# Optimization experiments

Measured on AMD Instinct MI355X. Metric: run time of the kernel, lower is better.

The kernel has to match this reference:

```python
import jax, jax.numpy as jnp
import numpy as np

B, H, W, C, HEADS, WS, SS = 32, 56, 56, 512, 16, 7, 3
HID = 4 * C
N = WS * WS          # tokens per window = 49
NW = (H // WS) * (W // WS)  # windows per image = 64
HD = C // HEADS
SCALE = HD ** -0.5

def _rel_index():
    coords = np.stack(np.meshgrid(np.arange(WS), np.arange(WS), indexing='ij'))
    cf = coords.reshape(2, -1)
    rel = (cf[:, :, None] - cf[:, None, :]).transpose(1, 2, 0)
    rel[..., 0] += WS - 1
    rel[..., 1] += WS - 1
    rel[..., 0] *= 2 * WS - 1
    return rel.sum(-1)  # [N, N]

REL_IDX = _rel_index()

def _attn_mask():
    # standard Swin SW-MSA mask: label 3x3 shifted regions, diff labels -> -100
    img = np.zeros((H, W), dtype=np.float32)
    cnt = 0
    for hs in (slice(0, -WS), slice(-WS, -SS), slice(-SS, None)):
        for ws_ in (slice(0, -WS), slice(-WS, -SS), slice(-SS, None)):
            img[hs, ws_] = cnt
            cnt += 1
    mw = img.reshape(H // WS, WS, W // WS, WS).transpose(0, 2, 1, 3).reshape(NW, N)
    diff = mw[:, None, :] - mw[:, :, None]
    return jnp.asarray(np.where(diff != 0, -100.0, 0.0).astype(np.float32))  # [NW, N, N]

ATTN_MASK = _attn_mask()

def layernorm(x, g, b, eps=1e-5):
    m = jnp.mean(x, -1, keepdims=True)
    v = jnp.mean((x - m) ** 2, -1, keepdims=True)
    return (x - m) * jax.lax.rsqrt(v + eps) * g + b

def setup_inputs():
    key = jax.random.key(0)
    ks = jax.random.split(key, 8)
    f32 = jnp.float32
    return {
        'x': jax.random.normal(ks[0], (B, H * W, C), f32),
        'norm1_g': jnp.ones((C,), f32), 'norm1_b': jnp.zeros((C,), f32),
        'qkv_w': jax.random.normal(ks[1], (3 * C, C), f32) * 0.02,
        'qkv_b': jnp.zeros((3 * C,), f32),
        'rel_bias': jax.random.normal(ks[2], ((2 * WS - 1) ** 2, HEADS), f32) * 0.02,
        'proj_w': jax.random.normal(ks[3], (C, C), f32) * 0.02,
        'proj_b': jnp.zeros((C,), f32),
        'norm2_g': jnp.ones((C,), f32), 'norm2_b': jnp.zeros((C,), f32),
        'mlp_w1': jax.random.normal(ks[4], (HID, C), f32) * 0.02,
        'mlp_b1': jnp.zeros((HID,), f32),
        'mlp_w2': jax.random.normal(ks[5], (C, HID), f32) * 0.02,
        'mlp_b2': jnp.zeros((C,), f32),
    }

def reference(x, norm1_g, norm1_b, qkv_w, qkv_b, rel_bias, proj_w, proj_b,
              norm2_g, norm2_b, mlp_w1, mlp_b1, mlp_w2, mlp_b2):
    skip = x
    h = layernorm(x, norm1_g, norm1_b).reshape(B, H, W, C)
    h = jnp.roll(h, (-SS, -SS), axis=(1, 2))  # cyclic shift
    # window partition -> [B*NW, N, C]
    h = h.reshape(B, H // WS, WS, W // WS, WS, C).transpose(0, 1, 3, 2, 4, 5).reshape(B * NW, N, C)
    qkv = (h @ qkv_w.T + qkv_b).reshape(B * NW, N, 3, HEADS, HD).transpose(2, 0, 3, 1, 4)
    q, k, v = qkv[0] * SCALE, qkv[1], qkv[2]  # [B*NW, HEADS, N, HD]
    attn = jnp.einsum('whnd,whmd->whnm', q, k)
    bias = rel_bias[REL_IDX.reshape(-1)].reshape(N, N, HEADS).transpose(2, 0, 1)
    attn = attn + bias[None]
    attn = attn.reshape(B, NW, HEADS, N, N) + ATTN_MASK[None, :, None]
    attn = jax.nn.softmax(attn, axis=-1).reshape(B * NW, HEADS, N, N)
    h = jnp.einsum('whnm,whmd->whnd', attn, v).transpose(0, 2, 1, 3).reshape(B * NW, N, C)
    h = h @ proj_w.T + proj_b
    # window reverse + reverse cyclic shift
    h = h.reshape(B, H // WS, W // WS, WS, WS, C).transpose(0, 1, 3, 2, 4, 5).reshape(B, H, W, C)
    h = jnp.roll(h, (SS, SS), axis=(1, 2)).reshape(B, H * W, C)
    x = skip + h
    m = layernorm(x, norm2_g, norm2_b)
    m = jax.nn.gelu(m @ mlp_w1.T + mlp_b1, approximate=False) @ mlp_w2.T + mlp_b2
    return x + m
```

## Files before the change

### kernel.cpp

```cpp
#include <hip/hip_runtime.h>
#include <cstdint>
#include <cstddef>

#define DI __device__ __forceinline__

typedef __bf16 bf16_t;
typedef __bf16 bf16x8 __attribute__((ext_vector_type(8)));
typedef float f32x4 __attribute__((ext_vector_type(4)));

static constexpr float SCALE = 0.17677669529663687f;

DI bf16_t f2b(float f) {
  uint32_t u = __builtin_bit_cast(uint32_t, f);
  u += 0x7fffu + ((u >> 16) & 1u);
  return __builtin_bit_cast(bf16_t, (uint16_t)(u >> 16));
}

DI void gld16(const void* g, void* l) {
  __builtin_amdgcn_global_load_lds(
      (const __attribute__((address_space(1))) uint32_t*)g,
      (__attribute__((address_space(3))) uint32_t*)l, 16, 0, 0);
}

__global__ __launch_bounds__(256)
void cvtw(const float* __restrict__ in, bf16_t* __restrict__ out, int n) {
  int i = (blockIdx.x * 256 + threadIdx.x) * 4;
  if (i >= n) return;
  float4 v = *(const float4*)(in + i);
  ushort4 o;
  o.x = __builtin_bit_cast(uint16_t, f2b(v.x));
  o.y = __builtin_bit_cast(uint16_t, f2b(v.y));
  o.z = __builtin_bit_cast(uint16_t, f2b(v.z));
  o.w = __builtin_bit_cast(uint16_t, f2b(v.w));
  *(ushort4*)(out + i) = o;
}

__global__ __launch_bounds__(256)
void bias_pre(const float* __restrict__ rel, float* __restrict__ bf) {
  int idx = blockIdx.x * 256 + threadIdx.x;
  int head = idx >> 12, t1 = (idx >> 6) & 63, t2 = idx & 63;
  float v = -1e30f;
  if (t1 < 49 && t2 < 49) {
    int i1 = t1 / 7, j1 = t1 - i1 * 7, i2 = t2 / 7, j2 = t2 - i2 * 7;
    v = rel[((i1 - i2 + 6) * 13 + (j1 - j2 + 6)) * 16 + head];
  }
  bf[idx] = v;
}

template<bool WIN>
__global__ __launch_bounds__(128)
void ln_kernel(const float* __restrict__ in, const float* __restrict__ g,
               const float* __restrict__ be, bf16_t* __restrict__ out)
{
  const int r = blockIdx.x;
  const int tid = threadIdx.x;
  long srow;
  if (WIN) {
    int bw = r / 49, t = r - bw * 49;
    int b = bw >> 6, w = bw & 63;
    int wh = w >> 3, ww = w & 7;
    int i = t / 7, j = t - i * 7;
    int hs = wh * 7 + i + 3; if (hs >= 56) hs -= 56;
    int wsr = ww * 7 + j + 3; if (wsr >= 56) wsr -= 56;
    srow = (long)b * 3136 + hs * 56 + wsr;
  } else {
    srow = r;
  }
  const float4 v = *(const float4*)(in + srow * 512 + tid * 4);
  float s = v.x + v.y + v.z + v.w;
  float sq = v.x * v.x + v.y * v.y + v.z * v.z + v.w * v.w;
#pragma unroll
  for (int m = 1; m < 64; m <<= 1) { s += __shfl_xor(s, m); sq += __shfl_xor(sq, m); }
  __shared__ float ls[2], lq[2];
  if ((tid & 63) == 0) { ls[tid >> 6] = s; lq[tid >> 6] = sq; }
  __syncthreads();
  s = ls[0] + ls[1]; sq = lq[0] + lq[1];
  const float mean = s * (1.f / 512.f);
  const float rs = rsqrtf(sq * (1.f / 512.f) - mean * mean + 1e-5f);
  const float4 gg = *(const float4*)(g + tid * 4);
  const float4 bb = *(const float4*)(be + tid * 4);
  ushort4 o;
  o.x = __builtin_bit_cast(uint16_t, f2b((v.x - mean) * rs * gg.x + bb.x));
  o.y = __builtin_bit_cast(uint16_t, f2b((v.y - mean) * rs * gg.y + bb.y));
  o.z = __builtin_bit_cast(uint16_t, f2b((v.z - mean) * rs * gg.z + bb.z));
  o.w = __builtin_bit_cast(uint16_t, f2b((v.w - mean) * rs * gg.w + bb.w));
  *(ushort4*)(out + (long)r * 512 + tid * 4) = o;
}

#define MFMA16(a, b, c) __builtin_amdgcn_mfma_f32_16x16x32_bf16((a), (b), (c), 0, 0, 0)

template<int EPI>
__global__ __launch_bounds__(512, 2)
void gemm256(const bf16_t* __restrict__ A, const bf16_t* __restrict__ Bw,
             const float* __restrict__ bias, const float* __restrict__ extra,
             void* __restrict__ out0, void* __restrict__ out1v, void* __restrict__ out2v,
             const int K, const int NBN)
{
  __shared__ __align__(128) bf16_t lds[8][8192];
  const int tid = threadIdx.x, lane = tid & 63, wave = tid >> 6;

  const int nwg = gridDim.x;
  const int q = nwg >> 3, r = nwg & 7;
  const int xcd = blockIdx.x & 7, sidx = blockIdx.x >> 3;
  const int wgid = (xcd < r ? xcd * (q + 1) : r * (q + 1) + (xcd - r) * q) + sidx;
  const int bm = wgid / NBN, bn = wgid - bm * NBN;

  const int srow = tid >> 2, slot = tid & 3;
  const int chunk = slot ^ ((srow >> 1) & 3);
  const bf16_t* pA = A + (size_t)(bm * 256 + srow) * K + chunk * 8;
  const bf16_t* pB = Bw + (size_t)(bn * 256 + srow) * K + chunk * 8;
  const size_t rowK = (size_t)128 * K;
  const int NT = K >> 6;

#define STG(mat, b, h, koff) do { \
    const bf16_t* _p = ((mat) ? pB : pA) + (koff); \
    bf16_t* _l = &lds[((mat) ? 4 : 0) + (b) * 2 + (h)][tid * 8]; \
    gld16(_p, _l); \
    gld16(_p + rowK, _l + 4096); \
  } while (0)

  STG(0, 0, 0, 0);  STG(1, 0, 0, 0);
  STG(0, 0, 1, 32); STG(1, 0, 1, 32);
  STG(0, 1, 0, 64); STG(1, 1, 0, 64);
  STG(0, 1, 1, 96);

  const int fr = lane & 15, fkc = lane >> 4;
  const int wr = wave >> 2, wc = wave & 3;
  const int slotq = (fkc ^ ((fr >> 1) & 3)) << 3;
  const int aoff = (wr * 128 + fr) * 32 + slotq;
  const int boff = (wc * 64 + fr) * 32 + slotq;

  f32x4 acc[8][4] = {};
  bf16x8 af[8], bq[4];

  asm volatile("s_waitcnt vmcnt(6)");
  __builtin_amdgcn_s_barrier();
  __builtin_amdgcn_sched_barrier(0);

#define PH_SYNC() \
  __builtin_amdgcn_sched_barrier(0); \
  __builtin_amdgcn_s_barrier(); \
  asm volatile("s_waitcnt lgkmcnt(0)"); \
  __builtin_amdgcn_sched_barrier(0); \
  __builtin_amdgcn_s_setprio(1)

#define PH_END() \
  __builtin_amdgcn_s_setprio(0); \
  __builtin_amdgcn_sched_barrier(0); \
  __builtin_amdgcn_s_barrier()

#define MM2(N0, N1) \
  _Pragma("unroll") \
  for (int m = 0; m < 8; ++m) { \
    acc[m][N0] = MFMA16(af[m], bq[N0], acc[m][N0]); \
    acc[m][N1] = MFMA16(af[m], bq[N1], acc[m][N1]); \
  }

#define KTILE(B, KT) do { \
     \
    _Pragma("unroll") \
    for (int m = 0; m < 8; ++m) af[m] = *(const bf16x8*)&lds[(B) * 2][aoff + m * 512]; \
    bq[0] = *(const bf16x8*)&lds[4 + (B) * 2][boff]; \
    bq[1] = *(const bf16x8*)&lds[4 + (B) * 2][boff + 512]; \
    if ((KT) + 1 < NT) STG(1, (B) ^ 1, 1, ((KT) + 1) * 64 + 32); \
    PH_SYNC(); \
    MM2(0, 1); \
    PH_END(); \
     \
    bq[2] = *(const bf16x8*)&lds[4 + (B) * 2][boff + 1024]; \
    bq[3] = *(const bf16x8*)&lds[4 + (B) * 2][boff + 1536]; \
    if ((KT) + 2 < NT) STG(0, (B), 0, ((KT) + 2) * 64); \
    PH_SYNC(); \
    MM2(2, 3); \
    PH_END(); \
     \
    _Pragma("unroll") \
    for (int m = 0; m < 8; ++m) af[m] = *(const bf16x8*)&lds[(B) * 2 + 1][aoff + m * 512]; \
    bq[0] = *(const bf16x8*)&lds[4 + (B) * 2 + 1][boff]; \
    bq[1] = *(const bf16x8*)&lds[4 + (B) * 2 + 1][boff + 512]; \
    if ((KT) + 2 < NT) STG(1, (B), 0, ((KT) + 2) * 64); \
    PH_SYNC(); \
    MM2(0, 1); \
    PH_END(); \
     \
    bq[2] = *(const bf16x8*)&lds[4 + (B) * 2 + 1][boff + 1024]; \
    bq[3] = *(const bf16x8*)&lds[4 + (B) * 2 + 1][boff + 1536]; \
    if ((KT) + 2 < NT) STG(0, (B), 1, ((KT) + 2) * 64 + 32); \
    PH_SYNC(); \
    MM2(2, 3); \
    __builtin_amdgcn_s_setprio(0); \
    __builtin_amdgcn_sched_barrier(0); \
    if ((KT) + 2 < NT) asm volatile("s_waitcnt vmcnt(6)"); \
    else               asm volatile("s_waitcnt vmcnt(0)"); \
    __builtin_amdgcn_s_barrier(); \
    __builtin_amdgcn_sched_barrier(0); \
  } while (0)

  for (int kt = 0; kt < NT; kt += 2) {
    KTILE(0, kt);
    KTILE(1, kt + 1);
  }
#undef KTILE
#undef MM2
#undef PH_END
#undef PH_SYNC
#undef STG

  const int rq = fkc * 4;
  float bs[4];
#pragma unroll
  for (int n = 0; n < 4; ++n) bs[n] = bias[bn * 256 + wc * 64 + n * 16 + fr];

#pragma unroll
  for (int m = 0; m < 8; ++m) {
#pragma unroll
    for (int j = 0; j < 4; ++j) {
      const int grow = bm * 256 + wr * 128 + m * 16 + rq + j;
      long obase = 0;
      if (EPI == 0) {
        int bwi = grow / 49, t = grow - bwi * 49;
        obase = ((long)bwi * 784 + t) * 32;
      } else if (EPI == 1) {
        int bwi = grow / 49, t = grow - bwi * 49;
        int b = bwi >> 6, w = bwi & 63;
        int wh = w >> 3, ww = w & 7;
        int i = t / 7, jj = t - i * 7;
        int hs = wh * 7 + i + 3; if (hs >= 56) hs -= 56;
        int wsr = ww * 7 + jj + 3; if (wsr >= 56) wsr -= 56;
        obase = ((long)b * 3136 + hs * 56 + wsr) * 512;
      } else if (EPI == 2) {
        obase = (long)grow * 2048;
      } else {
        obase = (long)grow * 512;
      }
#pragma unroll
      for (int n = 0; n < 4; ++n) {
        const int gcol = bn * 256 + wc * 64 + n * 16 + fr;
        float v = acc[m][n][j] + bs[n];
        if (EPI == 0) {
          int part = gcol >> 9, head = (gcol >> 5) & 15, d = gcol & 31;
          if (part == 0) v *= SCALE;
          bf16_t* dst = (bf16_t*)(part == 0 ? out0 : (part == 1 ? out1v : out2v));
          dst[obase + (long)head * 1568 + d] = f2b(v);
        } else if (EPI == 1) {
          ((float*)out0)[obase + gcol] = v + extra[obase + gcol];
        } else if (EPI == 2) {
          float m2 = v * v;
          float z = v * fmaf(0.07135481627f, m2, 1.59576912161f);
          float e = __expf(z);
          float rr = __builtin_amdgcn_rcpf(e + 1.0f);
          ((bf16_t*)out0)[obase + gcol] = f2b(fmaf(-v, rr, v));
        } else {
          ((float*)out0)[obase + gcol] = v + extra[obase + gcol];
        }
      }
    }
  }
}

__global__ __launch_bounds__(256)
void attn_kernel(const bf16_t* __restrict__ qb, const bf16_t* __restrict__ kb,
                 const bf16_t* __restrict__ vb, const float* __restrict__ biasf,
                 bf16_t* __restrict__ aout)
{
  __shared__ bf16_t Q[64 * 32];
  __shared__ bf16_t Kl[64 * 32];
  __shared__ bf16_t Vt[32 * 64];
  __shared__ bf16_t Pl[4][16 * 64];
  const int bid = blockIdx.x;
  const int bw = bid >> 4, head = bid & 15;
  const int tid = threadIdx.x, lane = tid & 63, wave = tid >> 6;
  {
    uint4 z = {0u, 0u, 0u, 0u};
    *(uint4*)&Q[tid * 8] = z;
    *(uint4*)&Kl[tid * 8] = z;
    *(uint4*)&Vt[tid * 8] = z;
  }
  __syncthreads();
  const bf16_t* qsrc = qb + (long)bid * (49 * 32);
  const bf16_t* ksrc = kb + (long)bid * (49 * 32);
  const bf16_t* vsrc = vb + (long)bid * (49 * 32);
  if (tid < 196) {
    *(uint4*)&Q[tid * 8] = *(const uint4*)(qsrc + tid * 8);
    *(uint4*)&Kl[tid * 8] = *(const uint4*)(ksrc + tid * 8);
  }
  for (int e = tid; e < 1568; e += 256) {
    int t = e >> 5, d = e & 31;
    Vt[d * 64 + t] = vsrc[e];
  }
  __syncthreads();
  const int fr = lane & 15, fk = (lane >> 4) * 8, rq = (lane >> 4) * 4;
  bf16x8 aq = *(const bf16x8*)&Q[(wave * 16 + fr) * 32 + fk];
  f32x4 s[4];
#pragma unroll
  for (int n = 0; n < 4; ++n) {
    bf16x8 bk = *(const bf16x8*)&Kl[(n * 16 + fr) * 32 + fk];
    f32x4 z = {0.f, 0.f, 0.f, 0.f};
    s[n] = __builtin_amdgcn_mfma_f32_16x16x32_bf16(aq, bk, z, 0, 0, 0);
  }
  const int w = bw & 63;
  const bool wh7 = ((w >> 3) == 7), ww7 = ((w & 7) == 7);
  const float* bh = biasf + head * 4096;
#pragma unroll
  for (int j = 0; j < 4; ++j) {
    const int row = wave * 16 + rq + j;
    int i1 = row / 7, j1 = row - i1 * 7;
    bool b1h = wh7 && (i1 >= 4), b1w = ww7 && (j1 >= 4);
    float pv[4];
    float mx = -3.0e38f;
#pragma unroll
    for (int n = 0; n < 4; ++n) {
      const int col = n * 16 + fr;
      float v = s[n][j] + bh[row * 64 + col];
      if (wh7 || ww7) {
        int i2 = col / 7, j2 = col - i2 * 7;
        bool b2h = wh7 && (i2 >= 4), b2w = ww7 && (j2 >= 4);
        if ((b1h != b2h) || (b1w != b2w)) v -= 100.f;
      }
      pv[n] = v;
      mx = fmaxf(mx, v);
    }
#pragma unroll
    for (int msk = 1; msk < 16; msk <<= 1) mx = fmaxf(mx, __shfl_xor(mx, msk));
    float sm = 0.f;
#pragma unroll
    for (int n = 0; n < 4; ++n) { pv[n] = __expf(pv[n] - mx); sm += pv[n]; }
#pragma unroll
    for (int msk = 1; msk < 16; msk <<= 1) sm += __shfl_xor(sm, msk);
    const float inv = 1.f / sm;
#pragma unroll
    for (int n = 0; n < 4; ++n)
      Pl[wave][(rq + j) * 64 + n * 16 + fr] = f2b(pv[n] * inv);
  }
  __syncthreads();
  f32x4 o[2] = {};
#pragma unroll
  for (int kk = 0; kk < 2; ++kk) {
    bf16x8 pa = *(const bf16x8*)&Pl[wave][fr * 64 + kk * 32 + fk];
#pragma unroll
    for (int dt = 0; dt < 2; ++dt) {
      bf16x8 vv = *(const bf16x8*)&Vt[(dt * 16 + fr) * 64 + kk * 32 + fk];
      o[dt] = __builtin_amdgcn_mfma_f32_16x16x32_bf16(pa, vv, o[dt], 0, 0, 0);
    }
  }
#pragma unroll
  for (int j = 0; j < 4; ++j) {
    const int t1 = wave * 16 + rq + j;
    if (t1 < 49) {
      bf16_t* dst = aout + ((long)bw * 49 + t1) * 512 + head * 32;
      dst[fr] = f2b(o[0][j]);
      dst[16 + fr] = f2b(o[1][j]);
    }
  }
}

extern "C" void kernel_launch(void* const* d_in, const int* in_sizes, int n_in,
                              void* d_out, int out_size, void* d_ws, size_t ws_size,
                              hipStream_t stream)
{
  const float* x      = (const float*)d_in[0];
  const float* n1g    = (const float*)d_in[1];
  const float* n1b    = (const float*)d_in[2];
  const float* qkv_w  = (const float*)d_in[3];
  const float* qkv_b  = (const float*)d_in[4];
  const float* rel    = (const float*)d_in[5];
  const float* proj_w = (const float*)d_in[6];
  const float* proj_b = (const float*)d_in[7];
  const float* n2g    = (const float*)d_in[8];
  const float* n2b    = (const float*)d_in[9];
  const float* w1     = (const float*)d_in[10];
  const float* b1     = (const float*)d_in[11];
  const float* w2     = (const float*)d_in[12];
  const float* b2     = (const float*)d_in[13];

  char* ws = (char*)d_ws;
  bf16_t* Wqkv  = (bf16_t*)(ws + 0);
  bf16_t* Wproj = (bf16_t*)(ws + 1572864);
  bf16_t* Wm1   = (bf16_t*)(ws + 2097152);
  bf16_t* Wm2   = (bf16_t*)(ws + 4194304);
  float*  biasf = (float*)(ws + 6291456);
  const size_t ABYTES = (size_t)100352 * 512 * 2;
  const size_t P1 = 8388608;
  const size_t P2 = P1 + ABYTES + 1048576;
  bf16_t* xw      = (bf16_t*)(ws + P1);
  bf16_t* qbuf    = (bf16_t*)(ws + P2);
  bf16_t* kbuf    = (bf16_t*)(ws + P2 + ABYTES);
  bf16_t* vbuf    = (bf16_t*)(ws + P2 + 2 * ABYTES);
  bf16_t* attnout = xw;
  bf16_t* h2      = xw;
  bf16_t* hidden  = qbuf;

  cvtw<<<768, 256, 0, stream>>>(qkv_w, Wqkv, 1536 * 512);
  cvtw<<<256, 256, 0, stream>>>(proj_w, Wproj, 512 * 512);
  cvtw<<<1024, 256, 0, stream>>>(w1, Wm1, 2048 * 512);
  cvtw<<<1024, 256, 0, stream>>>(w2, Wm2, 512 * 2048);
  bias_pre<<<256, 256, 0, stream>>>(rel, biasf);

  ln_kernel<true><<<100352, 128, 0, stream>>>(x, n1g, n1b, xw);
  gemm256<0><<<392 * 6, 512, 0, stream>>>(xw, Wqkv, qkv_b, nullptr,
                                          qbuf, kbuf, vbuf, 512, 6);
  attn_kernel<<<32768, 256, 0, stream>>>(qbuf, kbuf, vbuf, biasf, attnout);
  gemm256<1><<<392 * 2, 512, 0, stream>>>(attnout, Wproj, proj_b, x,
                                          d_out, nullptr, nullptr, 512, 2);
  ln_kernel<false><<<100352, 128, 0, stream>>>((const float*)d_out, n2g, n2b, h2);
  gemm256<2><<<392 * 8, 512, 0, stream>>>(h2, Wm1, b1, nullptr,
                                          hidden, nullptr, nullptr, 512, 8);
  gemm256<3><<<392 * 2, 512, 0, stream>>>(hidden, Wm2, b2, (const float*)d_out,
                                          d_out, nullptr, nullptr, 2048, 2);
}
```

Measured before the change: 1.356 ms.

## Make GEMMs persistent with contiguous tile ranges and cross-tile prefetch

All four GEMM launches now run a fixed grid of 256 workgroups, each taking a contiguous range of 256x256 output tiles mapped so that workgroups on the same XCD are adjacent. The LDS staging pipeline continues across tile boundaries, so loads for the next tile's K slices are issued while the current tile finishes and runs its epilogue. This targets wave-quantization tails and per-tile pipeline fill/drain. With launch bounds allowing 2 blocks per CU, 256 blocks may leave CUs idle, and the epilogue is serialized inside the loop.

```diff
diff --git a/kernel.cpp b/kernel.cpp
--- a/kernel.cpp
+++ b/kernel.cpp
@@ -98,31 +98,47 @@
 {
   __shared__ __align__(128) bf16_t lds[8][8192];
   const int tid = threadIdx.x, lane = tid & 63, wave = tid >> 6;
-
-  const int nwg = gridDim.x;
-  const int q = nwg >> 3, r = nwg & 7;
+  const int NT = K >> 6;
+  const int ntiles = NBN * 392;
+
   const int xcd = blockIdx.x & 7, sidx = blockIdx.x >> 3;
-  const int wgid = (xcd < r ? xcd * (q + 1) : r * (q + 1) + (xcd - r) * q) + sidx;
-  const int bm = wgid / NBN, bn = wgid - bm * NBN;
+  const int c = xcd * 32 + sidx;
+  const int q2 = ntiles >> 8, r2 = ntiles & 255;
+  const int t0 = c * q2 + (c < r2 ? c : r2);
+  const int t1 = t0 + q2 + (c < r2 ? 1 : 0);
 
   const int srow = tid >> 2, slot = tid & 3;
   const int chunk = slot ^ ((srow >> 1) & 3);
-  const bf16_t* pA = A + (size_t)(bm * 256 + srow) * K + chunk * 8;
-  const bf16_t* pB = Bw + (size_t)(bn * 256 + srow) * K + chunk * 8;
   const size_t rowK = (size_t)128 * K;
-  const int NT = K >> 6;
-
-#define STG(mat, b, h, koff) do { \
-    const bf16_t* _p = ((mat) ? pB : pA) + (koff); \
-    bf16_t* _l = &lds[((mat) ? 4 : 0) + (b) * 2 + (h)][tid * 8]; \
-    gld16(_p, _l); \
-    gld16(_p + rowK, _l + 4096); \
+  const size_t PANEL = (size_t)256 * K;
+
+  int bmC = t0 / NBN, bnC = t0 - bmC * NBN;
+
+  const bf16_t* pAs = A + (size_t)(bmC * 256 + srow) * K + chunk * 8;
+  const bf16_t* pBs = Bw + (size_t)(bnC * 256 + srow) * K + chunk * 8;
+  int hA = 0, hB = 0, ktA = 0, hhA = 0, bnA = bnC, ktB = 0, hhB = 0, bnB = bnC;
+  const int ST = (t1 - t0) * NT;
+  const int hEnd = ST * 2;
+
+#define STG_A() do { \
+    if (hA < hEnd) { \
+      const bf16_t* _p = pAs + ktA * 64 + hhA * 32; \
+      bf16_t* _l = &lds[(ktA & 1) * 2 + hhA][tid * 8]; \
+      gld16(_p, _l); gld16(_p + rowK, _l + 4096); \
+      ++hA; hhA ^= 1; \
+      if (!hhA) { if (++ktA == NT) { ktA = 0; if (++bnA == NBN) { bnA = 0; pAs += PANEL; } } } \
+    } \
   } while (0)
 
-  STG(0, 0, 0, 0);  STG(1, 0, 0, 0);
-  STG(0, 0, 1, 32); STG(1, 0, 1, 32);
-  STG(0, 1, 0, 64); STG(1, 1, 0, 64);
-  STG(0, 1, 1, 96);
+#define STG_B() do { \
+    if (hB < hEnd) { \
+      const bf16_t* _p = pBs + ktB * 64 + hhB * 32; \
+      bf16_t* _l = &lds[4 + (ktB & 1) * 2 + hhB][tid * 8]; \
+      gld16(_p, _l); gld16(_p + rowK, _l + 4096); \
+      ++hB; hhB ^= 1; \
+      if (!hhB) { if (++ktB == NT) { ktB = 0; pBs += PANEL; if (++bnB == NBN) { bnB = 0; pBs -= (size_t)NBN * PANEL; } } } \
+    } \
+  } while (0)
 
   const int fr = lane & 15, fkc = lane >> 4;
   const int wr = wave >> 2, wc = wave & 3;
@@ -133,6 +149,7 @@
   f32x4 acc[8][4] = {};
   bf16x8 af[8], bq[4];
 
+  STG_A(); STG_B(); STG_A(); STG_B(); STG_A(); STG_B(); STG_A();
   asm volatile("s_waitcnt vmcnt(6)");
   __builtin_amdgcn_s_barrier();
   __builtin_amdgcn_sched_barrier(0);
@@ -156,20 +173,20 @@
     acc[m][N1] = MFMA16(af[m], bq[N1], acc[m][N1]); \
   }
 
-#define KTILE(B, KT) do { \
+#define KTILE(B) do { \
      \
     _Pragma("unroll") \
     for (int m = 0; m < 8; ++m) af[m] = *(const bf16x8*)&lds[(B) * 2][aoff + m * 512]; \
     bq[0] = *(const bf16x8*)&lds[4 + (B) * 2][boff]; \
     bq[1] = *(const bf16x8*)&lds[4 + (B) * 2][boff + 512]; \
-    if ((KT) + 1 < NT) STG(1, (B) ^ 1, 1, ((KT) + 1) * 64 + 32); \
+    STG_B(); \
     PH_SYNC(); \
     MM2(0, 1); \
     PH_END(); \
      \
     bq[2] = *(const bf16x8*)&lds[4 + (B) * 2][boff + 1024]; \
     bq[3] = *(const bf16x8*)&lds[4 + (B) * 2][boff + 1536]; \
-    if ((KT) + 2 < NT) STG(0, (B), 0, ((KT) + 2) * 64); \
+    STG_A(); \
     PH_SYNC(); \
     MM2(2, 3); \
     PH_END(); \
@@ -178,84 +195,95 @@
     for (int m = 0; m < 8; ++m) af[m] = *(const bf16x8*)&lds[(B) * 2 + 1][aoff + m * 512]; \
     bq[0] = *(const bf16x8*)&lds[4 + (B) * 2 + 1][boff]; \
     bq[1] = *(const bf16x8*)&lds[4 + (B) * 2 + 1][boff + 512]; \
-    if ((KT) + 2 < NT) STG(1, (B), 0, ((KT) + 2) * 64); \
+    STG_B(); \
     PH_SYNC(); \
     MM2(0, 1); \
     PH_END(); \
      \
     bq[2] = *(const bf16x8*)&lds[4 + (B) * 2 + 1][boff + 1024]; \
     bq[3] = *(const bf16x8*)&lds[4 + (B) * 2 + 1][boff + 1536]; \
-    if ((KT) + 2 < NT) STG(0, (B), 1, ((KT) + 2) * 64 + 32); \
+    STG_A(); \
     PH_SYNC(); \
     MM2(2, 3); \
     __builtin_amdgcn_s_setprio(0); \
     __builtin_amdgcn_sched_barrier(0); \
-    if ((KT) + 2 < NT) asm volatile("s_waitcnt vmcnt(6)"); \
-    else               asm volatile("s_waitcnt vmcnt(0)"); \
+    if (sG + 2 < ST) asm volatile("s_waitcnt vmcnt(6)"); \
+    else             asm volatile("s_waitcnt vmcnt(0)"); \
     __builtin_amdgcn_s_barrier(); \
     __builtin_amdgcn_sched_barrier(0); \
+    ++sG; \
   } while (0)
 
-  for (int kt = 0; kt < NT; kt += 2) {
-    KTILE(0, kt);
-    KTILE(1, kt + 1);
+  int sG = 0;
+  const int rq = fkc * 4;
+  for (int t = t0; t < t1; ++t) {
+#pragma unroll 1
+    for (int k2 = 0; k2 < NT; k2 += 2) {
+      KTILE(0);
+      KTILE(1);
+    }
+    {
+      float bs[4];
+#pragma unroll
+      for (int n = 0; n < 4; ++n) bs[n] = bias[bnC * 256 + wc * 64 + n * 16 + fr];
+#pragma unroll
+      for (int m = 0; m < 8; ++m) {
+#pragma unroll
+        for (int j = 0; j < 4; ++j) {
+          const int grow = bmC * 256 + wr * 128 + m * 16 + rq + j;
+          long obase = 0;
+          if (EPI == 0) {
+            int bwi = grow / 49, t_ = grow - bwi * 49;
+            obase = ((long)bwi * 784 + t_) * 32;
+          } else if (EPI == 1) {
+            int bwi = grow / 49, t_ = grow - bwi * 49;
+            int b = bwi >> 6, w = bwi & 63;
+            int wh = w >> 3, ww = w & 7;
+            int i = t_ / 7, jj = t_ - i * 7;
+            int hs = wh * 7 + i + 3; if (hs >= 56) hs -= 56;
+            int wsr = ww * 7 + jj + 3; if (wsr >= 56) wsr -= 56;
+            obase = ((long)b * 3136 + hs * 56 + wsr) * 512;
+          } else if (EPI == 2) {
+            obase = (long)grow * 2048;
+          } else {
+            obase = (long)grow * 512;
+          }
+#pragma unroll
+          for (int n = 0; n < 4; ++n) {
+            const int gcol = bnC * 256 + wc * 64 + n * 16 + fr;
+            float v = acc[m][n][j] + bs[n];
+            if (EPI == 0) {
+              int part = gcol >> 9, head = (gcol >> 5) & 15, d = gcol & 31;
+              if (part == 0) v *= SCALE;
+              bf16_t* dst = (bf16_t*)(part == 0 ? out0 : (part == 1 ? out1v : out2v));
+              dst[obase + (long)head * 1568 + d] = f2b(v);
+            } else if (EPI == 1) {
+              ((float*)out0)[obase + gcol] = v + extra[obase + gcol];
+            } else if (EPI == 2) {
+              float m2 = v * v;
+              float z = v * fmaf(0.07135481627f, m2, 1.59576912161f);
+              float e = __expf(z);
+              float rr = __builtin_amdgcn_rcpf(e + 1.0f);
+              ((bf16_t*)out0)[obase + gcol] = f2b(fmaf(-v, rr, v));
+            } else {
+              ((float*)out0)[obase + gcol] = v + extra[obase + gcol];
+            }
+          }
+        }
+      }
+#pragma unroll
+      for (int m = 0; m < 8; ++m)
+#pragma unroll
+        for (int n = 0; n < 4; ++n) acc[m][n] = (f32x4){0.f, 0.f, 0.f, 0.f};
+    }
+    if (++bnC == NBN) { bnC = 0; ++bmC; }
   }
 #undef KTILE
 #undef MM2
 #undef PH_END
 #undef PH_SYNC
-#undef STG
-
-  const int rq = fkc * 4;
-  float bs[4];
-#pragma unroll
-  for (int n = 0; n < 4; ++n) bs[n] = bias[bn * 256 + wc * 64 + n * 16 + fr];
-
-#pragma unroll
-  for (int m = 0; m < 8; ++m) {
-#pragma unroll
-    for (int j = 0; j < 4; ++j) {
-      const int grow = bm * 256 + wr * 128 + m * 16 + rq + j;
-      long obase = 0;
-      if (EPI == 0) {
-        int bwi = grow / 49, t = grow - bwi * 49;
-        obase = ((long)bwi * 784 + t) * 32;
-      } else if (EPI == 1) {
-        int bwi = grow / 49, t = grow - bwi * 49;
-        int b = bwi >> 6, w = bwi & 63;
-        int wh = w >> 3, ww = w & 7;
-        int i = t / 7, jj = t - i * 7;
-        int hs = wh * 7 + i + 3; if (hs >= 56) hs -= 56;
-        int wsr = ww * 7 + jj + 3; if (wsr >= 56) wsr -= 56;
-        obase = ((long)b * 3136 + hs * 56 + wsr) * 512;
-      } else if (EPI == 2) {
-        obase = (long)grow * 2048;
-      } else {
-        obase = (long)grow * 512;
-      }
-#pragma unroll
-      for (int n = 0; n < 4; ++n) {
-        const int gcol = bn * 256 + wc * 64 + n * 16 + fr;
-        float v = acc[m][n][j] + bs[n];
-        if (EPI == 0) {
-          int part = gcol >> 9, head = (gcol >> 5) & 15, d = gcol & 31;
-          if (part == 0) v *= SCALE;
-          bf16_t* dst = (bf16_t*)(part == 0 ? out0 : (part == 1 ? out1v : out2v));
-          dst[obase + (long)head * 1568 + d] = f2b(v);
-        } else if (EPI == 1) {
-          ((float*)out0)[obase + gcol] = v + extra[obase + gcol];
-        } else if (EPI == 2) {
-          float m2 = v * v;
-          float z = v * fmaf(0.07135481627f, m2, 1.59576912161f);
-          float e = __expf(z);
-          float rr = __builtin_amdgcn_rcpf(e + 1.0f);
-          ((bf16_t*)out0)[obase + gcol] = f2b(fmaf(-v, rr, v));
-        } else {
-          ((float*)out0)[obase + gcol] = v + extra[obase + gcol];
-        }
-      }
-    }
-  }
+#undef STG_A
+#undef STG_B
 }
 
 __global__ __launch_bounds__(256)
@@ -397,14 +425,14 @@
   bias_pre<<<256, 256, 0, stream>>>(rel, biasf);
 
   ln_kernel<true><<<100352, 128, 0, stream>>>(x, n1g, n1b, xw);
-  gemm256<0><<<392 * 6, 512, 0, stream>>>(xw, Wqkv, qkv_b, nullptr,
-                                          qbuf, kbuf, vbuf, 512, 6);
+  gemm256<0><<<256, 512, 0, stream>>>(xw, Wqkv, qkv_b, nullptr,
+                                      qbuf, kbuf, vbuf, 512, 6);
   attn_kernel<<<32768, 256, 0, stream>>>(qbuf, kbuf, vbuf, biasf, attnout);
-  gemm256<1><<<392 * 2, 512, 0, stream>>>(attnout, Wproj, proj_b, x,
-                                          d_out, nullptr, nullptr, 512, 2);
+  gemm256<1><<<256, 512, 0, stream>>>(attnout, Wproj, proj_b, x,
+                                      d_out, nullptr, nullptr, 512, 2);
   ln_kernel<false><<<100352, 128, 0, stream>>>((const float*)d_out, n2g, n2b, h2);
-  gemm256<2><<<392 * 8, 512, 0, stream>>>(h2, Wm1, b1, nullptr,
-                                          hidden, nullptr, nullptr, 512, 8);
-  gemm256<3><<<392 * 2, 512, 0, stream>>>(hidden, Wm2, b2, (const float*)d_out,
-                                          d_out, nullptr, nullptr, 2048, 2);
-}
+  gemm256<2><<<256, 512, 0, stream>>>(h2, Wm1, b1, nullptr,
+                                      hidden, nullptr, nullptr, 512, 8);
+  gemm256<3><<<256, 512, 0, stream>>>(hidden, Wm2, b2, (const float*)d_out,
+                                      d_out, nullptr, nullptr, 2048, 2);
+}
```

Measured after the change: 1.410 ms. 4.0% more time.
